# Kernel optimization log

Measured on AMD Instinct MI355X. Metric: run time of the kernel, lower is better.

The kernel has to match this reference:

```python
import jax, jax.numpy as jnp
import numpy as np

N_EMBED = 1024
N_HEAD = 16
HEAD_DIM = N_EMBED // N_HEAD


def setup_inputs() -> dict:
    key = jax.random.key(0)
    ks = jax.random.split(key, 6)
    B, T, C = 4, 2048, N_EMBED
    scale = 1.0 / np.sqrt(C)
    x = jax.random.normal(ks[0], (B, T, C), dtype=jnp.float32)
    # torch nn.Linear weights are [out, in]; y = x @ W.T
    Wk = jax.random.normal(ks[1], (C, C), dtype=jnp.float32) * scale
    Wq = jax.random.normal(ks[2], (C, C), dtype=jnp.float32) * scale
    Wv = jax.random.normal(ks[3], (C, C), dtype=jnp.float32) * scale
    Wp = jax.random.normal(ks[4], (C, C), dtype=jnp.float32) * scale
    bp = jax.random.normal(ks[5], (C,), dtype=jnp.float32) * 0.01
    return {"x": x, "Wk": Wk, "Wq": Wq, "Wv": Wv, "Wp": Wp, "bp": bp}


def reference(x, Wk, Wq, Wv, Wp, bp):
    B, T, C = x.shape
    H, D = N_HEAD, HEAD_DIM
    # QKV projections (torch Linear: x @ W.T), split heads -> [B, H, T, D]
    k = (x @ Wk.T).reshape(B, T, H, D).transpose(0, 2, 1, 3)
    q = (x @ Wq.T).reshape(B, T, H, D).transpose(0, 2, 1, 3)
    v = (x @ Wv.T).reshape(B, T, H, D).transpose(0, 2, 1, 3)
    # scaled scores [B, H, T, T]
    att = jnp.einsum('bhtd,bhsd->bhts', q, k) * (1.0 / np.sqrt(D))
    causal = jnp.tril(jnp.ones((T, T), dtype=bool))
    att = jnp.where(causal[None, None, :, :], att, -jnp.inf)
    att = jax.nn.softmax(att, axis=-1)
    out = jnp.einsum('bhts,bhsd->bhtd', att, v)  # [B, H, T, D]
    out = out.transpose(0, 2, 1, 3).reshape(B, T, C)
    out = out @ Wp.T + bp
    return out
```

## Files before the change

### kernel.cpp

```cpp
#include <hip/hip_runtime.h>

typedef __bf16 bf16_t;
typedef bf16_t bf16x4 __attribute__((ext_vector_type(4)));
typedef bf16_t bf16x8 __attribute__((ext_vector_type(8)));
typedef float f32x4 __attribute__((ext_vector_type(4)));

#define B_ 4
#define T_ 2048
#define C_ 1024
#define H_ 16
#define D_ 64

#define GLDS(g, l)                                                          \
  __builtin_amdgcn_global_load_lds(                                         \
      (const __attribute__((address_space(1))) void*)(g),                   \
      (__attribute__((address_space(3))) void*)(l), 16, 0, 0)

static __device__ __forceinline__ f32x4 mfma16(bf16x8 a, bf16x8 b, f32x4 c) {
  return __builtin_amdgcn_mfma_f32_16x16x32_bf16(a, b, c, 0, 0, 0);
}

static __device__ __forceinline__ float exp2_hw(float x) {
  float r;
  asm("v_exp_f32 %0, %1" : "=v"(r) : "v"(x));
  return r;
}

__global__ void cvt_all(const float* __restrict__ x, const float* __restrict__ wq,
                        const float* __restrict__ wk, const float* __restrict__ wv,
                        const float* __restrict__ wp, bf16_t* __restrict__ xb,
                        bf16_t* __restrict__ wqb, bf16_t* __restrict__ wkb,
                        bf16_t* __restrict__ wvb, bf16_t* __restrict__ wpb) {
  int i = blockIdx.x * blockDim.x + threadIdx.x;
  const float* src;
  bf16_t* dst;
  int off;
  if (i < 2097152) {
    src = x; dst = xb; off = i;
  } else {
    int r = i - 2097152;
    int region = r >> 18;
    off = r & 262143;
    if (region == 0) { src = wq; dst = wqb; }
    else if (region == 1) { src = wk; dst = wkb; }
    else if (region == 2) { src = wv; dst = wvb; }
    else { src = wp; dst = wpb; }
  }
  float4 v = ((const float4*)src)[off];
  bf16x4 o = {(bf16_t)v.x, (bf16_t)v.y, (bf16_t)v.z, (bf16_t)v.w};
  ((bf16x4*)dst)[off] = o;
}

__global__ __launch_bounds__(512, 4) void gemm_qkv(
    const bf16_t* __restrict__ xb, const bf16_t* __restrict__ wq,
    const bf16_t* __restrict__ wk, const bf16_t* __restrict__ wv,
    bf16_t* __restrict__ qo, bf16_t* __restrict__ ko, bf16_t* __restrict__ vt) {
  __shared__ bf16_t lA[2][128 * 64];
  __shared__ bf16_t lB[2][3][64 * 64];
  const int tid = threadIdx.x, wave = tid >> 6, lane = tid & 63;
  const int g = lane >> 4;
  const int bid = blockIdx.x;
  const int swz = ((bid & 7) << 7) | (bid >> 3);
  const int col0 = (swz & 15) * 64, row0 = (swz >> 4) * 128;
  const int wr = wave >> 2, wc = wave & 3;
  f32x4 acc[3][4] = {};

  const int soffA[2] = {wave * 1024, (8 + wave) * 1024};
  size_t sgoA[2];
#pragma unroll
  for (int i = 0; i < 2; ++i) {
    const int lin = soffA[i] + lane * 16;
    const int r = lin >> 7;
    const int c = ((lin >> 4) & 7) ^ (r & 7);
    sgoA[i] = (size_t)r * C_ + c * 8;
  }
  const int soffB = wave * 1024;
  size_t sgoB;
  {
    const int lin = soffB + lane * 16;
    const int r = lin >> 7;
    const int c = ((lin >> 4) & 7) ^ (r & 7);
    sgoB = (size_t)r * C_ + c * 8;
  }
  int koffA[2][4], koffB[2];
#pragma unroll
  for (int s = 0; s < 2; ++s) {
    const int c = s * 4 + g;
#pragma unroll
    for (int m = 0; m < 4; ++m) {
      const int r = wr * 64 + m * 16 + (lane & 15);
      koffA[s][m] = r * 128 + ((c ^ (r & 7)) << 4);
    }
    const int rb = wc * 16 + (lane & 15);
    koffB[s] = rb * 128 + ((c ^ (rb & 7)) << 4);
  }

#define QKV_STAGE(k0, b)                                                    \
  {                                                                         \
    GLDS(xb + (size_t)row0 * C_ + (k0) + sgoA[0], &lA[b][soffA[0] >> 1]);   \
    GLDS(xb + (size_t)row0 * C_ + (k0) + sgoA[1], &lA[b][soffA[1] >> 1]);   \
    GLDS(wq + (size_t)col0 * C_ + (k0) + sgoB, &lB[b][0][soffB >> 1]);      \
    GLDS(wk + (size_t)col0 * C_ + (k0) + sgoB, &lB[b][1][soffB >> 1]);      \
    GLDS(wv + (size_t)col0 * C_ + (k0) + sgoB, &lB[b][2][soffB >> 1]);      \
  }

  QKV_STAGE(0, 0);
  int cur = 0;
  for (int k0 = 0; k0 < C_; k0 += 64) {
    __syncthreads();
    if (k0 + 64 < C_) QKV_STAGE(k0 + 64, cur ^ 1);
#pragma unroll
    for (int s = 0; s < 2; ++s) {
      const char* ab = (const char*)lA[cur];
      bf16x8 af[4];
#pragma unroll
      for (int m = 0; m < 4; ++m) af[m] = *(const bf16x8*)(ab + koffA[s][m]);
#pragma unroll
      for (int z = 0; z < 3; ++z) {
        bf16x8 bf = *(const bf16x8*)((const char*)lB[cur][z] + koffB[s]);
#pragma unroll
        for (int m = 0; m < 4; ++m) acc[z][m] = mfma16(af[m], bf, acc[z][m]);
      }
    }
    cur ^= 1;
  }
#pragma unroll
  for (int z = 0; z < 3; ++z) {
    bf16_t* outb = (z == 0) ? qo : ((z == 1) ? ko : vt);
    const float qs = (z == 0) ? 0.125f * 1.4426950408889634f : 1.0f;
    const int gc = col0 + wc * 16 + (lane & 15);
    const int h = gc >> 6, d = gc & 63;
#pragma unroll
    for (int m = 0; m < 4; ++m) {
      const int gr = row0 + wr * 64 + m * 16 + ((lane >> 4) << 2);
      const int b = gr >> 11, t = gr & (T_ - 1);
      if (z < 2) {
#pragma unroll
        for (int j = 0; j < 4; ++j)
          outb[(((size_t)(b * H_ + h)) * T_ + (t + j)) * D_ + d] =
              (bf16_t)(acc[z][m][j] * qs);
      } else {
        bf16x4 pk = {(bf16_t)acc[z][m][0], (bf16_t)acc[z][m][1],
                     (bf16_t)acc[z][m][2], (bf16_t)acc[z][m][3]};
        *(bf16x4*)(outb + (((size_t)(b * H_ + h)) * D_ + d) * T_ + t) = pk;
      }
    }
  }
}

__global__ __launch_bounds__(256) void gemm_proj(const bf16_t* __restrict__ att,
                                                 const bf16_t* __restrict__ wp,
                                                 const float* __restrict__ bias,
                                                 float* __restrict__ out) {
  __shared__ bf16_t lA[2][128 * 64];
  __shared__ bf16_t lB[2][128 * 64];
  const int tid = threadIdx.x;
  const int wave = tid >> 6, lane = tid & 63;
  const int wr = wave >> 1, wc = wave & 1;
  const int row0 = blockIdx.y * 128, col0 = blockIdx.x * 128;
  f32x4 acc[4][4] = {};

  const int soff[4] = {wave * 1024, (4 + wave) * 1024, (8 + wave) * 1024,
                       (12 + wave) * 1024};
  size_t sgo[4];
#pragma unroll
  for (int i = 0; i < 4; ++i) {
    const int lin = soff[i] + lane * 16;
    const int r = lin >> 7;
    const int c = ((lin >> 4) & 7) ^ (r & 7);
    sgo[i] = (size_t)r * C_ + c * 8;
  }

#define PROJ_STAGE(k0, b)                                                   \
  {                                                                         \
    _Pragma("unroll") for (int i = 0; i < 4; ++i) {                         \
      GLDS(att + (size_t)row0 * C_ + (k0) + sgo[i], &lA[b][soff[i] >> 1]);  \
      GLDS(wp + (size_t)col0 * C_ + (k0) + sgo[i], &lB[b][soff[i] >> 1]);   \
    }                                                                       \
  }

  PROJ_STAGE(0, 0);
  int cur = 0;
  for (int k0 = 0; k0 < C_; k0 += 64) {
    __syncthreads();
    if (k0 + 64 < C_) PROJ_STAGE(k0 + 64, cur ^ 1);
#pragma unroll
    for (int s = 0; s < 2; ++s) {
      bf16x8 af[4], bfr[4];
#pragma unroll
      for (int m = 0; m < 4; ++m) {
        const int r = wr * 64 + m * 16 + (lane & 15);
        const int c = s * 4 + (lane >> 4);
        af[m] = *(const bf16x8*)((const char*)lA[cur] + r * 128 +
                                 ((c ^ (r & 7)) << 4));
      }
#pragma unroll
      for (int n = 0; n < 4; ++n) {
        const int r = wc * 64 + n * 16 + (lane & 15);
        const int c = s * 4 + (lane >> 4);
        bfr[n] = *(const bf16x8*)((const char*)lB[cur] + r * 128 +
                                  ((c ^ (r & 7)) << 4));
      }
#pragma unroll
      for (int m = 0; m < 4; ++m)
#pragma unroll
        for (int n = 0; n < 4; ++n) acc[m][n] = mfma16(af[m], bfr[n], acc[m][n]);
    }
    cur ^= 1;
  }
#pragma unroll
  for (int m = 0; m < 4; ++m) {
#pragma unroll
    for (int n = 0; n < 4; ++n) {
      const int gr = row0 + wr * 64 + m * 16 + ((lane >> 4) << 2);
      const int gc = col0 + wc * 64 + n * 16 + (lane & 15);
      const float bv = bias[gc];
#pragma unroll
      for (int j = 0; j < 4; ++j)
        out[(size_t)(gr + j) * C_ + gc] = acc[m][n][j] + bv;
    }
  }
}

__global__ __launch_bounds__(512, 4) void attn_fwd(
    const bf16_t* __restrict__ Q, const bf16_t* __restrict__ K,
    const bf16_t* __restrict__ V, bf16_t* __restrict__ AO) {
  __shared__ bf16_t lK[2][2][64 * 64];
  __shared__ bf16_t lV[2][2][64 * 64];
  __shared__ bf16_t lP[8][16 * 64];
  const int tid = threadIdx.x, wave = tid >> 6, lane = tid & 63;
  const int g = lane >> 4;
  const int bh = blockIdx.y;
  const size_t baseK = (size_t)bh * T_ * D_;
  const size_t baseV = (size_t)bh * D_ * T_;
  const int bb = bh >> 4, hh = bh & 15;

  int koff[2][4];
#pragma unroll
  for (int s = 0; s < 2; ++s)
#pragma unroll
    for (int nf = 0; nf < 4; ++nf) {
      const int r = nf * 16 + (lane & 15);
      const int c = s * 4 + g;
      koff[s][nf] = r * 128 + ((c ^ (r & 7)) << 4);
    }
  int pwoff[4];
  {
    const int r = lane & 15;
#pragma unroll
    for (int nf = 0; nf < 4; ++nf)
      pwoff[nf] = r * 128 + (((2 * nf + (g >> 1)) ^ (r & 7)) << 4) +
                  ((g & 1) << 3);
  }
  const int soff = wave * 1024;
  const int slin = soff + lane * 16;
  const int srow = slin >> 7;
  const int scol = ((slin >> 4) & 7) ^ (srow & 7);
  const size_t kgo = (size_t)srow * D_ + scol * 8;
  const size_t vgo = (size_t)srow * T_ + scol * 8;

  for (int half = 0; half < 2; ++half) {
    const int qt = half ? (15 - blockIdx.x) : blockIdx.x;
    const int twv = qt * 128 + wave * 16;
    const int ntiles = qt + 1;
    __syncthreads();
#pragma unroll
    for (int sub = 0; sub < 2; ++sub) {
      GLDS(K + baseK + (size_t)sub * 64 * D_ + kgo, &lK[0][sub][soff >> 1]);
      GLDS(V + baseV + (size_t)sub * 64 + vgo, &lV[0][sub][soff >> 1]);
    }
    bf16x8 qf[2];
#pragma unroll
    for (int s = 0; s < 2; ++s)
      qf[s] = *(const bf16x8*)(Q + baseK +
                               (size_t)(twv + (lane & 15)) * D_ + s * 32 +
                               (g << 3));
    float lrun = 0.f;
    f32x4 o[4] = {};
    int cur = 0;
    for (int it = 0; it < ntiles; ++it) {
      __syncthreads();
      if (it + 1 < ntiles) {
        const int nb = cur ^ 1;
        const size_t ks = (size_t)(it + 1) * 128;
#pragma unroll
        for (int sub = 0; sub < 2; ++sub) {
          GLDS(K + baseK + (ks + sub * 64) * D_ + kgo,
               &lK[nb][sub][soff >> 1]);
          GLDS(V + baseV + ks + sub * 64 + vgo, &lV[nb][sub][soff >> 1]);
        }
      }
      const int s0 = it * 128;
      f32x4 sc[2][4];
#pragma unroll
      for (int sub = 0; sub < 2; ++sub)
#pragma unroll
        for (int nf = 0; nf < 4; ++nf) sc[sub][nf] = (f32x4){};
      __builtin_amdgcn_s_setprio(1);
#pragma unroll
      for (int sub = 0; sub < 2; ++sub) {
        const char* kb = (const char*)lK[cur][sub];
#pragma unroll
        for (int s = 0; s < 2; ++s)
#pragma unroll
          for (int nf = 0; nf < 4; ++nf)
            sc[sub][nf] =
                mfma16(*(const bf16x8*)(kb + koff[s][nf]), qf[s], sc[sub][nf]);
      }
      __builtin_amdgcn_s_setprio(0);
      if (it == qt) {
        const int t = twv + (lane & 15);
#pragma unroll
        for (int sub = 0; sub < 2; ++sub)
#pragma unroll
          for (int nf = 0; nf < 4; ++nf)
#pragma unroll
            for (int j = 0; j < 4; ++j) {
              const int s = s0 + sub * 64 + nf * 16 + g * 4 + j;
              if (s > t) sc[sub][nf][j] = -1e30f;
            }
      }
      float ps = 0.f;
      bf16x4 pk[2][4];
#pragma unroll
      for (int sub = 0; sub < 2; ++sub) {
        float psn[4];
#pragma unroll
        for (int nf = 0; nf < 4; ++nf) {
          float e0 = exp2_hw(sc[sub][nf][0]);
          float e1 = exp2_hw(sc[sub][nf][1]);
          float e2 = exp2_hw(sc[sub][nf][2]);
          float e3 = exp2_hw(sc[sub][nf][3]);
          pk[sub][nf][0] = (bf16_t)e0;
          pk[sub][nf][1] = (bf16_t)e1;
          pk[sub][nf][2] = (bf16_t)e2;
          pk[sub][nf][3] = (bf16_t)e3;
          psn[nf] = (e0 + e1) + (e2 + e3);
        }
        ps += (psn[0] + psn[1]) + (psn[2] + psn[3]);
      }
      ps += __shfl_xor(ps, 16);
      ps += __shfl_xor(ps, 32);
      lrun += ps;
      __builtin_amdgcn_s_setprio(1);
#pragma unroll
      for (int sub = 0; sub < 2; ++sub) {
        char* pw = (char*)lP[wave];
#pragma unroll
        for (int nf = 0; nf < 4; ++nf) *(bf16x4*)(pw + pwoff[nf]) = pk[sub][nf];
        const char* pb = (const char*)lP[wave];
        const char* vb = (const char*)lV[cur][sub];
#pragma unroll
        for (int s2 = 0; s2 < 2; ++s2) {
          bf16x8 pf = *(const bf16x8*)(pb + koff[s2][0]);
#pragma unroll
          for (int df = 0; df < 4; ++df)
            o[df] = mfma16(pf, *(const bf16x8*)(vb + koff[s2][df]), o[df]);
        }
      }
      __builtin_amdgcn_s_setprio(0);
      cur ^= 1;
    }
    {
      const float inv = 1.0f / lrun;
      float ib[4];
#pragma unroll
      for (int j = 0; j < 4; ++j)
        ib[j] = __shfl(inv, (lane & 48) | ((g << 2) + j));
#pragma unroll
      for (int j = 0; j < 4; ++j) {
        const int t = twv + (g << 2) + j;
#pragma unroll
        for (int df = 0; df < 4; ++df) {
          const int cc = hh * 64 + df * 16 + (lane & 15);
          AO[((size_t)(bb * T_ + t)) * C_ + cc] = (bf16_t)(o[df][j] * ib[j]);
        }
      }
    }
  }
}

extern "C" void kernel_launch(void* const* d_in, const int* in_sizes, int n_in,
                              void* d_out, int out_size, void* d_ws,
                              size_t ws_size, hipStream_t stream) {
  const float* x = (const float*)d_in[0];
  const float* Wk = (const float*)d_in[1];
  const float* Wq = (const float*)d_in[2];
  const float* Wv = (const float*)d_in[3];
  const float* Wp = (const float*)d_in[4];
  const float* bp = (const float*)d_in[5];
  char* ws = (char*)d_ws;
  bf16_t* xb = (bf16_t*)ws;
  bf16_t* wqb = (bf16_t*)(ws + (16u << 20));
  bf16_t* wkb = (bf16_t*)(ws + (18u << 20));
  bf16_t* wvb = (bf16_t*)(ws + (20u << 20));
  bf16_t* wpb = (bf16_t*)(ws + (22u << 20));
  bf16_t* q = (bf16_t*)(ws + (24u << 20));
  bf16_t* k = (bf16_t*)(ws + (40u << 20));
  bf16_t* vt = (bf16_t*)(ws + (56u << 20));
  bf16_t* att = xb;

  cvt_all<<<12288, 256, 0, stream>>>(x, Wq, Wk, Wv, Wp, xb, wqb, wkb, wvb, wpb);
  gemm_qkv<<<1024, 512, 0, stream>>>(xb, wqb, wkb, wvb, q, k, vt);
  attn_fwd<<<dim3(8, 64), 512, 0, stream>>>(q, k, vt, att);
  gemm_proj<<<dim3(8, 64), 256, 0, stream>>>(att, wpb, bp, (float*)d_out);
}
```

Measured before the change: 160.5 us.

## Retile output projection GEMM and compute softmax row sums with MFMA

The output projection GEMM moves from 512 blocks of 256 threads with 128x128 tiles to 1024 blocks of 512 threads with 128x64 tiles. Each wave now owns a 64x16 slice, and a swizzled block index improves L2 locality. Separately, the attention kernel drops its per-tile VALU sum of exponentials and cross-lane shuffles, and instead gets the row sums from an extra MFMA of P against a vector of ones. The aim is more parallelism and occupancy in the projection GEMM and less VALU and shuffle work in attention. The cost is lower per-wave reuse of operands in the GEMM, plus one extra MFMA per P fragment.

```diff
diff --git a/kernel.cpp b/kernel.cpp
--- a/kernel.cpp
+++ b/kernel.cpp
@@ -148,35 +148,55 @@
   }
 }
 
-__global__ __launch_bounds__(256) void gemm_proj(const bf16_t* __restrict__ att,
-                                                 const bf16_t* __restrict__ wp,
-                                                 const float* __restrict__ bias,
-                                                 float* __restrict__ out) {
+__global__ __launch_bounds__(512, 4) void gemm_proj(const bf16_t* __restrict__ att,
+                                                    const bf16_t* __restrict__ wp,
+                                                    const float* __restrict__ bias,
+                                                    float* __restrict__ out) {
   __shared__ bf16_t lA[2][128 * 64];
-  __shared__ bf16_t lB[2][128 * 64];
-  const int tid = threadIdx.x;
-  const int wave = tid >> 6, lane = tid & 63;
-  const int wr = wave >> 1, wc = wave & 1;
-  const int row0 = blockIdx.y * 128, col0 = blockIdx.x * 128;
-  f32x4 acc[4][4] = {};
-
-  const int soff[4] = {wave * 1024, (4 + wave) * 1024, (8 + wave) * 1024,
-                       (12 + wave) * 1024};
-  size_t sgo[4];
-#pragma unroll
-  for (int i = 0; i < 4; ++i) {
-    const int lin = soff[i] + lane * 16;
+  __shared__ bf16_t lB[2][64 * 64];
+  const int tid = threadIdx.x, wave = tid >> 6, lane = tid & 63;
+  const int g = lane >> 4;
+  const int bid = blockIdx.x;
+  const int swz = ((bid & 7) << 7) | (bid >> 3);
+  const int col0 = (swz & 15) * 64, row0 = (swz >> 4) * 128;
+  const int wr = wave >> 2, wc = wave & 3;
+  f32x4 acc[4] = {};
+
+  const int soffA[2] = {wave * 1024, (8 + wave) * 1024};
+  size_t sgoA[2];
+#pragma unroll
+  for (int i = 0; i < 2; ++i) {
+    const int lin = soffA[i] + lane * 16;
     const int r = lin >> 7;
     const int c = ((lin >> 4) & 7) ^ (r & 7);
-    sgo[i] = (size_t)r * C_ + c * 8;
+    sgoA[i] = (size_t)r * C_ + c * 8;
+  }
+  const int soffB = wave * 1024;
+  size_t sgoB;
+  {
+    const int lin = soffB + lane * 16;
+    const int r = lin >> 7;
+    const int c = ((lin >> 4) & 7) ^ (r & 7);
+    sgoB = (size_t)r * C_ + c * 8;
+  }
+  int koffA[2][4], koffB[2];
+#pragma unroll
+  for (int s = 0; s < 2; ++s) {
+    const int c = s * 4 + g;
+#pragma unroll
+    for (int m = 0; m < 4; ++m) {
+      const int r = wr * 64 + m * 16 + (lane & 15);
+      koffA[s][m] = r * 128 + ((c ^ (r & 7)) << 4);
+    }
+    const int rb = wc * 16 + (lane & 15);
+    koffB[s] = rb * 128 + ((c ^ (rb & 7)) << 4);
   }
 
 #define PROJ_STAGE(k0, b)                                                   \
   {                                                                         \
-    _Pragma("unroll") for (int i = 0; i < 4; ++i) {                         \
-      GLDS(att + (size_t)row0 * C_ + (k0) + sgo[i], &lA[b][soff[i] >> 1]);  \
-      GLDS(wp + (size_t)col0 * C_ + (k0) + sgo[i], &lB[b][soff[i] >> 1]);   \
-    }                                                                       \
+    GLDS(att + (size_t)row0 * C_ + (k0) + sgoA[0], &lA[b][soffA[0] >> 1]);  \
+    GLDS(att + (size_t)row0 * C_ + (k0) + sgoA[1], &lA[b][soffA[1] >> 1]);  \
+    GLDS(wp + (size_t)col0 * C_ + (k0) + sgoB, &lB[b][soffB >> 1]);         \
   }
 
   PROJ_STAGE(0, 0);
@@ -186,39 +206,24 @@
     if (k0 + 64 < C_) PROJ_STAGE(k0 + 64, cur ^ 1);
 #pragma unroll
     for (int s = 0; s < 2; ++s) {
-      bf16x8 af[4], bfr[4];
-#pragma unroll
-      for (int m = 0; m < 4; ++m) {
-        const int r = wr * 64 + m * 16 + (lane & 15);
-        const int c = s * 4 + (lane >> 4);
-        af[m] = *(const bf16x8*)((const char*)lA[cur] + r * 128 +
-                                 ((c ^ (r & 7)) << 4));
-      }
-#pragma unroll
-      for (int n = 0; n < 4; ++n) {
-        const int r = wc * 64 + n * 16 + (lane & 15);
-        const int c = s * 4 + (lane >> 4);
-        bfr[n] = *(const bf16x8*)((const char*)lB[cur] + r * 128 +
-                                  ((c ^ (r & 7)) << 4));
-      }
-#pragma unroll
-      for (int m = 0; m < 4; ++m)
-#pragma unroll
-        for (int n = 0; n < 4; ++n) acc[m][n] = mfma16(af[m], bfr[n], acc[m][n]);
+      const char* ab = (const char*)lA[cur];
+      bf16x8 af[4];
+#pragma unroll
+      for (int m = 0; m < 4; ++m) af[m] = *(const bf16x8*)(ab + koffA[s][m]);
+      bf16x8 bf = *(const bf16x8*)((const char*)lB[cur] + koffB[s]);
+#pragma unroll
+      for (int m = 0; m < 4; ++m) acc[m] = mfma16(af[m], bf, acc[m]);
     }
     cur ^= 1;
   }
+  const int gc = col0 + wc * 16 + (lane & 15);
+  const float bv = bias[gc];
 #pragma unroll
   for (int m = 0; m < 4; ++m) {
-#pragma unroll
-    for (int n = 0; n < 4; ++n) {
-      const int gr = row0 + wr * 64 + m * 16 + ((lane >> 4) << 2);
-      const int gc = col0 + wc * 64 + n * 16 + (lane & 15);
-      const float bv = bias[gc];
-#pragma unroll
-      for (int j = 0; j < 4; ++j)
-        out[(size_t)(gr + j) * C_ + gc] = acc[m][n][j] + bv;
-    }
+    const int gr = row0 + wr * 64 + m * 16 + ((lane >> 4) << 2);
+#pragma unroll
+    for (int j = 0; j < 4; ++j)
+      out[(size_t)(gr + j) * C_ + gc] = acc[m][j] + bv;
   }
 }
 
@@ -235,6 +240,10 @@
   const size_t baseV = (size_t)bh * D_ * T_;
   const int bb = bh >> 4, hh = bh & 15;
 
+  bf16x8 vones;
+#pragma unroll
+  for (int e = 0; e < 8; ++e) vones[e] = (bf16_t)1.0f;
+
   int koff[2][4];
 #pragma unroll
   for (int s = 0; s < 2; ++s)
@@ -275,7 +284,7 @@
       qf[s] = *(const bf16x8*)(Q + baseK +
                                (size_t)(twv + (lane & 15)) * D_ + s * 32 +
                                (g << 3));
-    float lrun = 0.f;
+    f32x4 lacc = {};
     f32x4 o[4] = {};
     int cur = 0;
     for (int it = 0; it < ntiles; ++it) {
@@ -320,28 +329,16 @@
               if (s > t) sc[sub][nf][j] = -1e30f;
             }
       }
-      float ps = 0.f;
       bf16x4 pk[2][4];
 #pragma unroll
-      for (int sub = 0; sub < 2; ++sub) {
-        float psn[4];
+      for (int sub = 0; sub < 2; ++sub)
 #pragma unroll
         for (int nf = 0; nf < 4; ++nf) {
-          float e0 = exp2_hw(sc[sub][nf][0]);
-          float e1 = exp2_hw(sc[sub][nf][1]);
-          float e2 = exp2_hw(sc[sub][nf][2]);
-          float e3 = exp2_hw(sc[sub][nf][3]);
-          pk[sub][nf][0] = (bf16_t)e0;
-          pk[sub][nf][1] = (bf16_t)e1;
-          pk[sub][nf][2] = (bf16_t)e2;
-          pk[sub][nf][3] = (bf16_t)e3;
-          psn[nf] = (e0 + e1) + (e2 + e3);
+          pk[sub][nf][0] = (bf16_t)exp2_hw(sc[sub][nf][0]);
+          pk[sub][nf][1] = (bf16_t)exp2_hw(sc[sub][nf][1]);
+          pk[sub][nf][2] = (bf16_t)exp2_hw(sc[sub][nf][2]);
+          pk[sub][nf][3] = (bf16_t)exp2_hw(sc[sub][nf][3]);
         }
-        ps += (psn[0] + psn[1]) + (psn[2] + psn[3]);
-      }
-      ps += __shfl_xor(ps, 16);
-      ps += __shfl_xor(ps, 32);
-      lrun += ps;
       __builtin_amdgcn_s_setprio(1);
 #pragma unroll
       for (int sub = 0; sub < 2; ++sub) {
@@ -353,6 +350,7 @@
 #pragma unroll
         for (int s2 = 0; s2 < 2; ++s2) {
           bf16x8 pf = *(const bf16x8*)(pb + koff[s2][0]);
+          lacc = mfma16(pf, vones, lacc);
 #pragma unroll
           for (int df = 0; df < 4; ++df)
             o[df] = mfma16(pf, *(const bf16x8*)(vb + koff[s2][df]), o[df]);
@@ -362,18 +360,14 @@
       cur ^= 1;
     }
     {
-      const float inv = 1.0f / lrun;
-      float ib[4];
-#pragma unroll
-      for (int j = 0; j < 4; ++j)
-        ib[j] = __shfl(inv, (lane & 48) | ((g << 2) + j));
 #pragma unroll
       for (int j = 0; j < 4; ++j) {
+        const float inv = 1.0f / lacc[j];
         const int t = twv + (g << 2) + j;
 #pragma unroll
         for (int df = 0; df < 4; ++df) {
           const int cc = hh * 64 + df * 16 + (lane & 15);
-          AO[((size_t)(bb * T_ + t)) * C_ + cc] = (bf16_t)(o[df][j] * ib[j]);
+          AO[((size_t)(bb * T_ + t)) * C_ + cc] = (bf16_t)(o[df][j] * inv);
         }
       }
     }
@@ -403,5 +397,5 @@
   cvt_all<<<12288, 256, 0, stream>>>(x, Wq, Wk, Wv, Wp, xb, wqb, wkb, wvb, wpb);
   gemm_qkv<<<1024, 512, 0, stream>>>(xb, wqb, wkb, wvb, q, k, vt);
   attn_fwd<<<dim3(8, 64), 512, 0, stream>>>(q, k, vt, att);
-  gemm_proj<<<dim3(8, 64), 256, 0, stream>>>(att, wpb, bp, (float*)d_out);
-}
+  gemm_proj<<<1024, 512, 0, stream>>>(att, wpb, bp, (float*)d_out);
+}
```

Measured after the change: 165.0 us. +2.8%, slower.
